# Kernel tuning notes

Hardware: AMD Instinct MI355X
Metric: run time of the kernel (lower is better)

Reference implementation:

```python
import jax, jax.numpy as jnp
from jax import lax
import numpy as np

GZ = 15.0   # grid extent (float, from gz=15.0)
G = 15      # grid cells per axis


def _disty(p):
    # p: [B, N, 3] points in [0, GZ). 12 features per point:
    # offsets to cell center / lower corner / upper corner (9) + their euclidean norms (3)
    c = jnp.floor(jnp.clip(p, 0.0, GZ - 1e-4))
    off_c = p - (c + 0.5)
    off_l = p - c
    off_u = p - (c + 1.0)
    norms = jnp.stack([jnp.sqrt((o * o).sum(-1)) for o in (off_c, off_l, off_u)], axis=-1)
    return jnp.concatenate([off_c, off_l, off_u, norms], axis=-1)  # [B, N, 12]


def _mlp(x, W1, b1, W2, b2, W3, b3):
    h = jax.nn.elu(x @ W1 + b1)
    h = jax.nn.elu(h @ W2 + b2)
    return h @ W3 + b3  # [B, N, 4]


def _agg(feats, p):
    # scatter-max per-point features into the [G,G,G] grid of each scene
    B, N, C = feats.shape
    cell = jnp.floor(jnp.clip(p, 0.0, GZ - 1e-4)).astype(jnp.int32)  # [B, N, 3]
    flat = (cell[..., 0] * G + cell[..., 1]) * G + cell[..., 2]
    flat = flat + (jnp.arange(B, dtype=jnp.int32) * (G ** 3))[:, None]
    grid = jnp.zeros((B * G ** 3, C), feats.dtype)
    grid = grid.at[flat.reshape(-1)].max(feats.reshape(-1, C))
    return grid.reshape(B, G, G, G, C).transpose(0, 4, 1, 2, 3)  # [B, 4, G, G, G]


def _conv_bn_elu(x, w, b, g, beta, stride):
    y = lax.conv_general_dilated(x, w, (stride,) * 3, [(2, 2)] * 3,
                                 dimension_numbers=('NCDHW', 'OIDHW', 'NCDHW'))
    y = y + b[None, :, None, None, None]
    # BatchNorm3d, training mode (batch statistics), eps=1e-5
    m = y.mean((0, 2, 3, 4), keepdims=True)
    v = ((y - m) ** 2).mean((0, 2, 3, 4), keepdims=True)
    y = (y - m) * lax.rsqrt(v + 1e-5)
    y = y * g[None, :, None, None, None] + beta[None, :, None, None, None]
    return jax.nn.elu(y)


def setup_inputs():
    key = jax.random.key(0)
    ks = jax.random.split(key, 16)
    B, N = 4, 300000
    pts = lambda k: jax.random.uniform(k, (B, N, 3), jnp.float32, 0.0, GZ)
    lin = lambda k, i, o: (jax.random.normal(k, (i, o), jnp.float32) / np.sqrt(i)).astype(jnp.float32)
    inp = {
        'goals': pts(ks[0]), 'inputs': pts(ks[1]), 'backgrounds': pts(ks[2]),
        'W1': lin(ks[3], 12, 16), 'b1': jnp.zeros((16,), jnp.float32),
        'W2': lin(ks[4], 16, 16), 'b2': jnp.zeros((16,), jnp.float32),
        'W3': lin(ks[5], 16, 4),  'b3': jnp.zeros((4,), jnp.float32),
        'conv1_w': (jax.random.normal(ks[6], (8, 12, 5, 5, 5), jnp.float32) / np.sqrt(12 * 125)).astype(jnp.float32),
        'conv1_b': jnp.zeros((8,), jnp.float32),
        'bn1_g': jnp.ones((8,), jnp.float32), 'bn1_b': jnp.zeros((8,), jnp.float32),
        'convs_w': (jax.random.normal(ks[7], (6, 8, 8, 5, 5, 5), jnp.float32) / np.sqrt(8 * 125)).astype(jnp.float32),
        'convs_b': jnp.zeros((6, 8), jnp.float32),
        'bns_g': jnp.ones((6, 8), jnp.float32), 'bns_b': jnp.zeros((6, 8), jnp.float32),
    }
    return inp


def reference(goals, inputs, backgrounds, W1, b1, W2, b2, W3, b3,
              conv1_w, conv1_b, bn1_g, bn1_b, convs_w, convs_b, bns_g, bns_b):
    def encode(p):
        return _agg(_mlp(_disty(p), W1, b1, W2, b2, W3, b3), p)

    scenes = jnp.concatenate([encode(inputs), encode(goals), encode(backgrounds)], axis=1)  # [B,12,G,G,G]
    x = _conv_bn_elu(scenes, conv1_w, conv1_b, bn1_g, bn1_b, 2)  # [B,8,8,8,8]
    for i in range(6):
        x = _conv_bn_elu(x, convs_w[i], convs_b[i], bns_g[i], bns_b[i], 1)
    return x
```

## Files before the change

### kernel.cpp

```cpp
#include <hip/hip_runtime.h>
#include <math.h>

#define B 4
#define NPTS 300000
#define G 15
#define G3 3375
#define PAIR_FLOATS (4*G3)
#define SCENE_FLOATS (B*12*G3)

typedef float v2f __attribute__((ext_vector_type(2)));

__device__ __forceinline__ float eluf(float v) {
    return v > 0.0f ? v : __expf(v) - 1.0f;
}

__global__ __launch_bounds__(128)
void prep_kernel(const float* __restrict__ W1, const float* __restrict__ b1,
                 float* __restrict__ W1f, float* __restrict__ b1f,
                 float* __restrict__ stats)
{
    int t = threadIdx.x;
    stats[t] = 0.0f;
    if (t < 16) {
        int j = t;
#pragma unroll
        for (int d = 0; d < 3; ++d) {
            W1f[d * 16 + j] = W1[d * 16 + j] + W1[(d + 3) * 16 + j]
                            + W1[(d + 6) * 16 + j];
            W1f[(3 + d) * 16 + j] = W1[(9 + d) * 16 + j];
        }
        float acc = 0.0f;
#pragma unroll
        for (int d = 0; d < 3; ++d)
            acc += W1[(d + 3) * 16 + j] - W1[(d + 6) * 16 + j];
        b1f[j] = b1[j] + 0.5f * acc;
    }
}

__global__ __launch_bounds__(256)
void mlp_kernel(const float* __restrict__ P0,
                const float* __restrict__ P1,
                const float* __restrict__ P2,
                const float* __restrict__ W1f, const float* __restrict__ b1f,
                const float* __restrict__ W2, const float* __restrict__ b2,
                const float* __restrict__ W3, const float* __restrict__ b3,
                float4* __restrict__ vals, unsigned short* __restrict__ cells,
                int s0, int m)
{
    int b   = blockIdx.y;
    int set = blockIdx.z;
    int i   = blockIdx.x * 256 + threadIdx.x;
    if (i >= m) return;
    const float* P = (set == 0) ? P0 : ((set == 1) ? P1 : P2);

    const float* p = P + ((size_t)b * NPTS + (size_t)(s0 + i)) * 3;
    float px = p[0], py = p[1], pz = p[2];

    const float HI = 14.9999f;
    float cx = floorf(fminf(fmaxf(px, 0.0f), HI));
    float cy = floorf(fminf(fmaxf(py, 0.0f), HI));
    float cz = floorf(fminf(fmaxf(pz, 0.0f), HI));

    float ox = px - (cx + 0.5f);
    float oy = py - (cy + 0.5f);
    float oz = pz - (cz + 0.5f);
    float nc2 = ox*ox + oy*oy + oz*oz;
    float s3  = ox + oy + oz;
    float in6[6];
    in6[0] = ox; in6[1] = oy; in6[2] = oz;
    in6[3] = sqrtf(nc2);
    in6[4] = sqrtf(nc2 + s3 + 0.75f);
    in6[5] = sqrtf(nc2 - s3 + 0.75f);

    float h1[16];
#pragma unroll
    for (int j = 0; j < 16; ++j) {
        float s = b1f[j];
#pragma unroll
        for (int k = 0; k < 6; ++k) s = fmaf(in6[k], W1f[k * 16 + j], s);
        h1[j] = eluf(s);
    }

    const v2f* W2v = (const v2f*)W2;
    const v2f* W3v = (const v2f*)W3;
    const v2f* b2v = (const v2f*)b2;
    const v2f* b3v = (const v2f*)b3;

    float h2[16];
#pragma unroll
    for (int j2 = 0; j2 < 8; ++j2) {
        v2f s = b2v[j2];
#pragma unroll
        for (int k = 0; k < 16; ++k) {
            v2f xb; xb.x = h1[k]; xb.y = h1[k];
            s = xb * W2v[k * 8 + j2] + s;
        }
        h2[2*j2]   = eluf(s.x);
        h2[2*j2+1] = eluf(s.y);
    }
    v2f o01 = b3v[0], o23 = b3v[1];
#pragma unroll
    for (int k = 0; k < 16; ++k) {
        v2f xb; xb.x = h2[k]; xb.y = h2[k];
        o01 = xb * W3v[k * 2 + 0] + o01;
        o23 = xb * W3v[k * 2 + 1] + o23;
    }

    int cell = (((int)cx) * G + (int)cy) * G + (int)cz;
    int pair = b * 3 + set;
    vals [(size_t)pair * m + i] = make_float4(o01.x, o01.y, o23.x, o23.y);
    cells[(size_t)pair * m + i] = (unsigned short)cell;
}

__global__ __launch_bounds__(512)
void scatter_kernel(const float4* __restrict__ vals,
                    const unsigned short* __restrict__ cells,
                    float* __restrict__ scenesR, int K, int m, int carry)
{
    __shared__ unsigned sg[PAIR_FLOATS];

    int rep = blockIdx.x;
    int b   = blockIdx.y;
    int set = blockIdx.z;
    int pair = b * 3 + set;
    float* myrep = scenesR + ((size_t)pair * K + rep) * PAIR_FLOATS;

    if (carry) {
        for (int i = threadIdx.x; i < PAIR_FLOATS; i += 512)
            sg[i] = __float_as_uint(myrep[i]);
    } else {
        for (int i = threadIdx.x; i < PAIR_FLOATS; i += 512)
            sg[i] = 0u;
    }
    __syncthreads();

    int chunk = (m + K - 1) / K;
    int start = rep * chunk;
    int end   = min(m, start + chunk);
    const float4*         v = vals  + (size_t)pair * m;
    const unsigned short* c = cells + (size_t)pair * m;

    for (int i = start + (int)threadIdx.x; i < end; i += 512) {
        float4 o = v[i];
        int cell = c[i];
        if (o.x > 0.0f) atomicMax(&sg[          cell], __float_as_uint(o.x));
        if (o.y > 0.0f) atomicMax(&sg[    G3 + cell], __float_as_uint(o.y));
        if (o.z > 0.0f) atomicMax(&sg[2 * G3 + cell], __float_as_uint(o.z));
        if (o.w > 0.0f) atomicMax(&sg[3 * G3 + cell], __float_as_uint(o.w));
    }
    __syncthreads();

    for (int i = threadIdx.x; i < PAIR_FLOATS; i += 512)
        myrep[i] = __uint_as_float(sg[i]);
}

__global__ __launch_bounds__(256)
void reduce_kernel(const float* __restrict__ scenesR, float* __restrict__ scenes,
                   int K)
{
    int t = blockIdx.x * 256 + threadIdx.x;
    if (t >= SCENE_FLOATS) return;
    int pair = t / PAIR_FLOATS;
    int j    = t - pair * PAIR_FLOATS;
    const float* src = scenesR + (size_t)pair * K * PAIR_FLOATS + j;
    float mx = 0.0f;
    for (int r = 0; r < K; ++r)
        mx = fmaxf(mx, src[(size_t)r * PAIR_FLOATS]);
    scenes[t] = mx;
}

__global__ __launch_bounds__(768)
void conv1_kernel(const float* __restrict__ scenes,
                  const float* __restrict__ w,
                  const float* __restrict__ bias,
                  float* __restrict__ y, float* __restrict__ stats)
{
    __shared__ float sred[768];
    int bx = blockIdx.x;
    int od = bx & 7, co = (bx >> 3) & 7, b = bx >> 6;
    int tid = threadIdx.x;
    int ow = tid & 7, oh = (tid >> 3) & 7, ci = tid >> 6;

    const float* sc = scenes + (size_t)(b * 12 + ci) * G3;
    const float* wc = w + (size_t)(co * 12 + ci) * 125;
    float s = 0.0f;
#pragma unroll
    for (int kd = 0; kd < 5; ++kd) {
        int id = od * 2 - 2 + kd;
        if ((unsigned)id >= (unsigned)G) continue;
#pragma unroll
        for (int kh = 0; kh < 5; ++kh) {
            int ih = oh * 2 - 2 + kh;
            bool hok = (unsigned)ih < (unsigned)G;
#pragma unroll
            for (int kw = 0; kw < 5; ++kw) {
                int iw = ow * 2 - 2 + kw;
                if (hok && (unsigned)iw < (unsigned)G)
                    s = fmaf(sc[(id * G + ih) * G + iw], wc[kd*25 + kh*5 + kw], s);
            }
        }
    }
    sred[tid] = s;
    __syncthreads();
    if (tid < 64) {
        float tot = bias[co];
#pragma unroll
        for (int g2 = 0; g2 < 12; ++g2) tot += sred[g2 * 64 + tid];
        y[(size_t)(b * 8 + co) * 512 + od * 64 + tid] = tot;
        float sum = tot, sq = tot * tot;
#pragma unroll
        for (int o = 32; o > 0; o >>= 1) {
            sum += __shfl_down(sum, o, 64);
            sq  += __shfl_down(sq,  o, 64);
        }
        if (tid == 0) { atomicAdd(&stats[co], sum); atomicAdd(&stats[8 + co], sq); }
    }
}

__global__ __launch_bounds__(512)
void conv_s_kernel(const float* __restrict__ yin,
                   const float* __restrict__ w,
                   const float* __restrict__ bias,
                   const float* __restrict__ g, const float* __restrict__ bet,
                   const float* __restrict__ stats_in,
                   float* __restrict__ yout, float* __restrict__ stats_out)
{
    __shared__ float slab[8 * 5 * 144];
    __shared__ float sstat[16], sscale[8], sshift[8];
    __shared__ float sred[512];

    int bx = blockIdx.x;
    int od = bx & 7, co = (bx >> 3) & 7, b = bx >> 6;
    int tid = threadIdx.x;

    float raw[8];
#pragma unroll
    for (int k = 0; k < 8; ++k) {
        int r = k * 512 + tid;
        raw[k] = yin[((size_t)(b * 8) << 9) + r];
    }

    if (tid < 16) sstat[tid] = stats_in[tid];
    for (int i = tid; i < 5760; i += 512) slab[i] = 0.0f;
    __syncthreads();

    if (tid < 8) {
        float S = sstat[tid], Q = sstat[8 + tid];
        float m  = S * (1.0f / 2048.0f);
        float vv = Q * (1.0f / 2048.0f) - m * m;
        float rs = rsqrtf(vv + 1e-5f);
        float sc = g[tid] * rs;
        sscale[tid] = sc;
        sshift[tid] = bet[tid] - m * sc;
    }
    __syncthreads();

#pragma unroll
    for (int k = 0; k < 8; ++k) {
        int r  = k * 512 + tid;
        int ci = r >> 9, rem = r & 511;
        int id = rem >> 6, ih = (rem >> 3) & 7, iw = rem & 7;
        int kd = id - od + 2;
        if ((unsigned)kd < 5u) {
            float t = fmaf(raw[k], sscale[ci], sshift[ci]);
            slab[ci * 720 + kd * 144 + (ih + 2) * 12 + (iw + 2)] =
                t > 0.0f ? t : __expf(t) - 1.0f;
        }
    }
    __syncthreads();

    int ow = tid & 7, oh = (tid >> 3) & 7, ci = tid >> 6;
    const float* sl = slab + ci * 720;
    const float* wc = w + (size_t)(co * 8 + ci) * 125;
    float s = 0.0f;
#pragma unroll
    for (int kd = 0; kd < 5; ++kd) {
#pragma unroll
        for (int kh = 0; kh < 5; ++kh) {
            const float* row = sl + kd * 144 + (oh + kh) * 12 + ow;
            const float* wr = wc + kd * 25 + kh * 5;
#pragma unroll
            for (int kw = 0; kw < 5; ++kw) s = fmaf(row[kw], wr[kw], s);
        }
    }
    sred[tid] = s;
    __syncthreads();
    if (tid < 64) {
        float tot = bias[co];
#pragma unroll
        for (int g2 = 0; g2 < 8; ++g2) tot += sred[g2 * 64 + tid];
        yout[(size_t)(b * 8 + co) * 512 + od * 64 + tid] = tot;
        float sum = tot, sq = tot * tot;
#pragma unroll
        for (int o = 32; o > 0; o >>= 1) {
            sum += __shfl_down(sum, o, 64);
            sq  += __shfl_down(sq,  o, 64);
        }
        if (tid == 0) { atomicAdd(&stats_out[co], sum); atomicAdd(&stats_out[8 + co], sq); }
    }
}

__global__ __launch_bounds__(256)
void bn_final_kernel(const float* __restrict__ yin,
                     const float* __restrict__ g, const float* __restrict__ bet,
                     const float* __restrict__ stats_in, float* __restrict__ outp)
{
    int i = blockIdx.x * 256 + threadIdx.x;
    float v = yin[i];
    int c = (i >> 9) & 7;
    float S = stats_in[c], Q = stats_in[8 + c];
    float m  = S * (1.0f / 2048.0f);
    float vv = Q * (1.0f / 2048.0f) - m * m;
    float rs = rsqrtf(vv + 1e-5f);
    float sc = g[c] * rs;
    float sh = bet[c] - m * sc;
    float t = fmaf(v, sc, sh);
    outp[i] = t > 0.0f ? t : __expf(t) - 1.0f;
}

extern "C" void kernel_launch(void* const* d_in, const int* in_sizes, int n_in,
                              void* d_out, int out_size, void* d_ws, size_t ws_size,
                              hipStream_t stream)
{
    const float* goals       = (const float*)d_in[0];
    const float* inputs      = (const float*)d_in[1];
    const float* backgrounds = (const float*)d_in[2];
    const float* W1 = (const float*)d_in[3];
    const float* b1 = (const float*)d_in[4];
    const float* W2 = (const float*)d_in[5];
    const float* b2 = (const float*)d_in[6];
    const float* W3 = (const float*)d_in[7];
    const float* b3 = (const float*)d_in[8];
    const float* conv1_w = (const float*)d_in[9];
    const float* conv1_b = (const float*)d_in[10];
    const float* bn1_g   = (const float*)d_in[11];
    const float* bn1_b   = (const float*)d_in[12];
    const float* convs_w = (const float*)d_in[13];
    const float* convs_b = (const float*)d_in[14];
    const float* bns_g   = (const float*)d_in[15];
    const float* bns_b   = (const float*)d_in[16];

    long ws_floats = (long)(ws_size / 4);
    long fixed = SCENE_FLOATS + 2L * 16384 + 256;
    static const int plans[][2] = {
        {42,1},{42,2},{42,4},{24,4},{21,6},{16,8},{8,12},{4,16},{2,32},{1,64}};
    int K = 1, S = 64;
    for (int pi = 0; pi < 10; ++pi) {
        int pk = plans[pi][0], ps = plans[pi][1];
        long mseg = (NPTS + ps - 1) / ps;
        long need = 54L * mseg + (long)pk * SCENE_FLOATS + fixed;
        if (need <= ws_floats) { K = pk; S = ps; break; }
    }
    int Mseg = (NPTS + S - 1) / S;

    float*          wsp     = (float*)d_ws;
    float4*         vals    = (float4*)wsp;
    unsigned short* cells   = (unsigned short*)(wsp + 48L * Mseg);
    float*          scenesR = wsp + 54L * Mseg;
    float*          scenes  = scenesR + (size_t)K * SCENE_FLOATS;
    float*          yA      = scenes + SCENE_FLOATS;
    float*          yB      = yA + 16384;
    float*          stats   = yB + 16384;
    float*          W1f     = stats + 128;
    float*          b1f     = W1f + 96;

    prep_kernel<<<1, 128, 0, stream>>>(W1, b1, W1f, b1f, stats);

    for (int s = 0; s < S; ++s) {
        int s0 = s * Mseg;
        int m  = min(Mseg, NPTS - s0);
        dim3 agrid((m + 255) / 256, B, 3);
        mlp_kernel<<<agrid, 256, 0, stream>>>(inputs, goals, backgrounds,
                                              W1f, b1f, W2, b2, W3, b3,
                                              vals, cells, s0, m);
        dim3 bgrid(K, B, 3);
        scatter_kernel<<<bgrid, 512, 0, stream>>>(vals, cells, scenesR, K, m,
                                                  s > 0 ? 1 : 0);
    }

    reduce_kernel<<<(SCENE_FLOATS + 255) / 256, 256, 0, stream>>>(scenesR, scenes, K);

    conv1_kernel<<<256, 768, 0, stream>>>(scenes, conv1_w, conv1_b, yA, stats);

    const float* cur = yA;
    float* nxt = yB;
    for (int i = 0; i < 6; ++i) {
        const float* g   = (i == 0) ? bn1_g : (bns_g + (i - 1) * 8);
        const float* bet = (i == 0) ? bn1_b : (bns_b + (i - 1) * 8);
        conv_s_kernel<<<256, 512, 0, stream>>>(
            cur, convs_w + (size_t)i * 8000, convs_b + i * 8,
            g, bet, stats + i * 16, nxt, stats + (i + 1) * 16);
        const float* tmp = cur; cur = nxt; nxt = (float*)tmp;
    }

    bn_final_kernel<<<64, 256, 0, stream>>>(cur, bns_g + 5 * 8, bns_b + 5 * 8,
                                            stats + 6 * 16, (float*)d_out);
}
```

Baseline: 278.2 us.

## Split scatter-max into two channel halves to halve LDS and double blocks

Stores the MLP outputs as two float2 planes instead of one float4 array, and splits the scatter kernel so each block handles only two of the four feature channels. Each block now needs half the shared-memory grid, which should allow more resident blocks per CU, and the grid has twice as many blocks. In exchange, cell indices are read twice and the reduction kernel indexes the replicas through the new half layout.

```diff
diff --git a/kernel.cpp b/kernel.cpp
--- a/kernel.cpp
+++ b/kernel.cpp
@@ -6,6 +6,7 @@
 #define G 15
 #define G3 3375
 #define PAIR_FLOATS (4*G3)
+#define HALF_FLOATS (2*G3)
 #define SCENE_FLOATS (B*12*G3)
 
 typedef float v2f __attribute__((ext_vector_type(2)));
@@ -44,7 +45,8 @@
                 const float* __restrict__ W1f, const float* __restrict__ b1f,
                 const float* __restrict__ W2, const float* __restrict__ b2,
                 const float* __restrict__ W3, const float* __restrict__ b3,
-                float4* __restrict__ vals, unsigned short* __restrict__ cells,
+                float2* __restrict__ vals01, float2* __restrict__ vals23,
+                unsigned short* __restrict__ cells,
                 int s0, int m)
 {
     int b   = blockIdx.y;
@@ -108,28 +110,29 @@
 
     int cell = (((int)cx) * G + (int)cy) * G + (int)cz;
     int pair = b * 3 + set;
-    vals [(size_t)pair * m + i] = make_float4(o01.x, o01.y, o23.x, o23.y);
-    cells[(size_t)pair * m + i] = (unsigned short)cell;
+    vals01[(size_t)pair * m + i] = make_float2(o01.x, o01.y);
+    vals23[(size_t)pair * m + i] = make_float2(o23.x, o23.y);
+    cells [(size_t)pair * m + i] = (unsigned short)cell;
 }
 
 __global__ __launch_bounds__(512)
-void scatter_kernel(const float4* __restrict__ vals,
+void scatter_kernel(const float2* __restrict__ vals01,
+                    const float2* __restrict__ vals23,
                     const unsigned short* __restrict__ cells,
                     float* __restrict__ scenesR, int K, int m, int carry)
 {
-    __shared__ unsigned sg[PAIR_FLOATS];
-
-    int rep = blockIdx.x;
-    int b   = blockIdx.y;
-    int set = blockIdx.z;
-    int pair = b * 3 + set;
-    float* myrep = scenesR + ((size_t)pair * K + rep) * PAIR_FLOATS;
+    __shared__ unsigned sg[HALF_FLOATS];
+
+    int rep  = blockIdx.x;
+    int pair = blockIdx.y;
+    int half = blockIdx.z;
+    float* myrep = scenesR + (((size_t)pair * K + rep) * 2 + half) * HALF_FLOATS;
 
     if (carry) {
-        for (int i = threadIdx.x; i < PAIR_FLOATS; i += 512)
+        for (int i = threadIdx.x; i < HALF_FLOATS; i += 512)
             sg[i] = __float_as_uint(myrep[i]);
     } else {
-        for (int i = threadIdx.x; i < PAIR_FLOATS; i += 512)
+        for (int i = threadIdx.x; i < HALF_FLOATS; i += 512)
             sg[i] = 0u;
     }
     __syncthreads();
@@ -137,20 +140,18 @@
     int chunk = (m + K - 1) / K;
     int start = rep * chunk;
     int end   = min(m, start + chunk);
-    const float4*         v = vals  + (size_t)pair * m;
+    const float2*         v = (half ? vals23 : vals01) + (size_t)pair * m;
     const unsigned short* c = cells + (size_t)pair * m;
 
     for (int i = start + (int)threadIdx.x; i < end; i += 512) {
-        float4 o = v[i];
+        float2 o = v[i];
         int cell = c[i];
-        if (o.x > 0.0f) atomicMax(&sg[          cell], __float_as_uint(o.x));
-        if (o.y > 0.0f) atomicMax(&sg[    G3 + cell], __float_as_uint(o.y));
-        if (o.z > 0.0f) atomicMax(&sg[2 * G3 + cell], __float_as_uint(o.z));
-        if (o.w > 0.0f) atomicMax(&sg[3 * G3 + cell], __float_as_uint(o.w));
-    }
-    __syncthreads();
-
-    for (int i = threadIdx.x; i < PAIR_FLOATS; i += 512)
+        if (o.x > 0.0f) atomicMax(&sg[     cell], __float_as_uint(o.x));
+        if (o.y > 0.0f) atomicMax(&sg[G3 + cell], __float_as_uint(o.y));
+    }
+    __syncthreads();
+
+    for (int i = threadIdx.x; i < HALF_FLOATS; i += 512)
         myrep[i] = __uint_as_float(sg[i]);
 }
 
@@ -162,7 +163,9 @@
     if (t >= SCENE_FLOATS) return;
     int pair = t / PAIR_FLOATS;
     int j    = t - pair * PAIR_FLOATS;
-    const float* src = scenesR + (size_t)pair * K * PAIR_FLOATS + j;
+    int half = j / HALF_FLOATS;
+    int jj   = j - half * HALF_FLOATS;
+    const float* src = scenesR + (((size_t)pair * K) * 2 + half) * HALF_FLOATS + jj;
     float mx = 0.0f;
     for (int r = 0; r < K; ++r)
         mx = fmaxf(mx, src[(size_t)r * PAIR_FLOATS]);
@@ -354,7 +357,8 @@
     int Mseg = (NPTS + S - 1) / S;
 
     float*          wsp     = (float*)d_ws;
-    float4*         vals    = (float4*)wsp;
+    float2*         vals01  = (float2*)wsp;
+    float2*         vals23  = (float2*)(wsp + 24L * Mseg);
     unsigned short* cells   = (unsigned short*)(wsp + 48L * Mseg);
     float*          scenesR = wsp + 54L * Mseg;
     float*          scenes  = scenesR + (size_t)K * SCENE_FLOATS;
@@ -372,9 +376,10 @@
         dim3 agrid((m + 255) / 256, B, 3);
         mlp_kernel<<<agrid, 256, 0, stream>>>(inputs, goals, backgrounds,
                                               W1f, b1f, W2, b2, W3, b3,
-                                              vals, cells, s0, m);
-        dim3 bgrid(K, B, 3);
-        scatter_kernel<<<bgrid, 512, 0, stream>>>(vals, cells, scenesR, K, m,
+                                              vals01, vals23, cells, s0, m);
+        dim3 bgrid(K, 12, 2);
+        scatter_kernel<<<bgrid, 512, 0, stream>>>(vals01, vals23, cells,
+                                                  scenesR, K, m,
                                                   s > 0 ? 1 : 0);
     }
 
```

Result: no change. 278.2 us (+0.0%).
